# Performance work log

Hardware: AMD Instinct MI355X
Metric: run time of the kernel (lower is better)

The kernel has to match this reference:

```python
import jax, jax.numpy as jnp
import numpy as np

HEAD = 8

def _mvn(x, eps=1e-5):
    # per-(batch,channel) mean/std over spatial dims; torch .var default is unbiased (ddof=1)
    mean = jnp.mean(x, axis=(2, 3), keepdims=True)
    var = jnp.var(x, axis=(2, 3), ddof=1, keepdims=True) + eps
    return (x - mean) / jnp.sqrt(var)

def _conv1x1(x, w, b):
    return jnp.einsum('bchw,oc->bohw', x, w) + b[None, :, None, None]

def _block_heads(x, p):
    # non-overlapping unfold (kernel==stride==p): pure reshape; matches torch unfold ordering
    b, c, h, w = x.shape
    y = x.reshape(b, c, h // p, p, w // p, p).transpose(0, 1, 2, 4, 3, 5)
    n, r = (h // p) * (w // p), p * p
    return y.reshape(b, HEAD, c // HEAD, n, r)

def _unblock(x, p, h, w):
    # inverse of non-overlapping unfold (fold with kernel==stride)
    b, c, n, r = x.shape
    y = x.reshape(b, c, h // p, w // p, p, p).transpose(0, 1, 2, 4, 3, 5)
    return y.reshape(b, c, h, w)

def setup_inputs() -> dict:
    key = jax.random.key(0)
    ks = jax.random.split(key, 12)
    B, C, H, W = 4, 512, 64, 64
    wmat = lambda k: jax.random.normal(k, (C, C), jnp.float32) * 0.05
    zb = jnp.zeros((C,), jnp.float32)
    return {
        'content': jax.random.normal(ks[0], (B, C, H, W), jnp.float32),
        'style': jax.random.normal(ks[1], (B, C, H, W), jnp.float32),
        'q_w': wmat(ks[2]), 'q_b': zb,
        'k_w': wmat(ks[3]), 'k_b': zb,
        'v_w': wmat(ks[4]), 'v_b': zb,
        'q2_w': wmat(ks[5]), 'q2_b': zb,
        'k2_w': wmat(ks[6]), 'k2_b': zb,
        'v2_w': wmat(ks[7]), 'v2_b': zb,
        'f1_w': wmat(ks[8]), 'f1_b': zb,
        'f2_w': wmat(ks[9]), 'f2_b': zb,
        'sim_alpha': jnp.ones((1,), jnp.float32),
        'sim_beta': jnp.zeros((1,), jnp.float32),
        'layer': 3,
    }

def reference(content, style, q_w, q_b, k_w, k_b, v_w, v_b, q2_w, q2_b, k2_w, k2_b,
              v2_w, v2_b, f1_w, f1_b, f2_w, f2_b, sim_alpha, sim_beta, layer):
    region = 8 if int(layer) in (3, 4) else 4
    b, c, h, w = content.shape
    nc = _mvn(content)
    ns = _mvn(style)
    DA_q = _block_heads(_conv1x1(nc, q_w, q_b), region)      # [b,H,ch,n,r]
    DA_k = _block_heads(_conv1x1(ns, k_w, k_b), region)
    DA_v = _block_heads(_conv1x1(style, v_w, v_b), region)
    PA_q = _block_heads(_conv1x1(nc, q2_w, q2_b), region)
    PA_k = _block_heads(_conv1x1(ns, k2_w, k2_b), region)
    PA_v = _block_heads(_conv1x1(style, v2_w, v2_b), region)
    r = region * region
    n = DA_q.shape[3]
    # --- distinctiveness attention: mean-center clustering + sigmoid-weighted aggregation ---
    DA_k_c = jnp.mean(DA_k, axis=-1)                          # [b,H,ch,n]
    DA_v_c = jnp.mean(DA_v, axis=-1)
    dis = jnp.einsum('bhcx,bhcxy->bhxy', DA_k_c, DA_k)
    sim = jax.nn.sigmoid(sim_beta + sim_alpha * dis)          # [b,H,n,r]
    DA_k_agg = (jnp.einsum('bhxy,bhcxy->bhcx', sim, DA_k) + DA_k_c) / (r + 1)
    DA_v_agg = (jnp.einsum('bhxy,bhcxy->bhcx', sim, DA_v) + DA_v_c) / (r + 1)
    logits = jnp.einsum('bhcxy,bhcz->bhyxz', DA_q, DA_k_agg)  # [b,H,r,n,n]
    scores = jax.nn.softmax(logits, axis=-1)
    DA = jnp.einsum('bhyxz,bhcz->bhcxy', scores, DA_v_agg)    # [b,H,ch,n,r]
    DA_ub = _unblock(DA.reshape(b, c, n, r), region, h, w)
    # --- point attention: argmax NN block matching, then intra-block attention ---
    PA1 = jnp.einsum('bhcxy,bhczy->bhxz', PA_q, PA_k)         # [b,H,n,n]
    idx = jnp.argmax(PA1, axis=-1)                            # [b,H,n]
    idx_b = jnp.broadcast_to(idx[:, :, None, :, None], PA_k.shape)
    PA_k_rs = jnp.take_along_axis(PA_k, idx_b, axis=3)
    PA_v_rs = jnp.take_along_axis(PA_v, idx_b, axis=3)
    logits2 = jnp.einsum('bhcxy,bhcxz->bhxyz', PA_q, PA_k_rs) # [b,H,n,r,r]
    scores2 = jax.nn.softmax(logits2, axis=-1)
    PA = jnp.einsum('bhxyz,bhcxz->bhcxy', scores2, PA_v_rs)
    PA_ub = _unblock(PA.reshape(b, c, n, r), region, h, w)
    O = _conv1x1(DA_ub, f1_w, f1_b) + _conv1x1(PA_ub, f2_w, f2_b)
    return O + content
```

## Files before the change

### kernel.cpp

```cpp
#include <hip/hip_runtime.h>

typedef unsigned short u16;
typedef unsigned int   u32;
typedef _Float16       f16;

typedef f16   f16x8 __attribute__((ext_vector_type(8)));
typedef f16   f16x4 __attribute__((ext_vector_type(4)));
typedef float f32x4 __attribute__((ext_vector_type(4)));

__device__ __forceinline__ f32x4 mfma16(f16x8 a, f16x8 b, f32x4 c){
  return __builtin_amdgcn_mfma_f32_16x16x32_f16(a, b, c, 0, 0, 0);
}

__device__ __forceinline__ void glds16(const f16* g, f16* l){
  __builtin_amdgcn_global_load_lds(
      (const __attribute__((address_space(1))) void*)g,
      (__attribute__((address_space(3))) void*)l, 16, 0, 0);
}

__device__ __forceinline__ void barrier_f(){
  __builtin_amdgcn_s_barrier();
  asm volatile("" ::: "memory");
}

// ... 9 lines not shown
  for(int i = t * 4; i < 4096; i += 1024){
    float4 v = *(const float4*)(xp + i);
    s  += (double)v.x + (double)v.y + (double)v.z + (double)v.w;
    ss += (double)v.x * v.x + (double)v.y * v.y + (double)v.z * v.z + (double)v.w * v.w;
  }
  #pragma unroll
  for(int off = 32; off > 0; off >>= 1){
    s  += __shfl_xor(s, off);
    ss += __shfl_xor(ss, off);
  }
  __shared__ double sh[8];
  const int wid = t >> 6;
  if((t & 63) == 0){ sh[wid] = s; sh[4 + wid] = ss; }
  __syncthreads();
  if(t == 0){
    double S  = sh[0] + sh[1] + sh[2] + sh[3];
    double SS = sh[4] + sh[5] + sh[6] + sh[7];
    float mean = (float)(S * (1.0 / 4096.0));
    float var  = (float)((SS - S * S * (1.0 / 4096.0)) * (1.0 / 4095.0));
    stats[src * 4096 + row] = mean;
    stats[src * 4096 + 2048 + row] = rsqrtf(var + 1e-5f);
  }
}

__global__ __launch_bounds__(256) void k_prep_w_all(
    const float* __restrict__ qW,  const float* __restrict__ qB,
    const float* __restrict__ kW,  const float* __restrict__ kB,
    const float* __restrict__ q2W, const float* __restrict__ q2B,
    const float* __restrict__ k2W, const float* __restrict__ k2B,
    const float* __restrict__ vW,  const float* __restrict__ vB,
    const float* __restrict__ v2W, const float* __restrict__ v2B,
    const float* __restrict__ f1W, const float* __restrict__ f2W,
    const float* __restrict__ stats,
    f16* __restrict__ qw, f16* __restrict__ kw,
    f16* __restrict__ q2wh, f16* __restrict__ q2wl,
    f16* __restrict__ k2wh, f16* __restrict__ k2wl,
    f16* __restrict__ vw, f16* __restrict__ v2w,
    f16* __restrict__ f1w, f16* __restrict__ f2w,
    float* __restrict__ biasp)
{
  const int t = threadIdx.x;
  int rid = blockIdx.x * 32 + (t >> 3);
  const float *W; const float *B = nullptr;
  int side = -1, b = 0, o;
  f16 *oh; f16 *ol = nullptr; float* bs = nullptr;
  if(rid < 2048){
    b = rid >> 9; o = rid & 511;
    W = qW; B = qB; side = 0;
    oh = qw + (size_t)(b * 512 + o) * 512;
    bs = biasp + 0 * 2048 + b * 512 + o;
  } else if(rid < 4096){
    rid -= 2048; b = rid >> 9; o = rid & 511;
    W = kW; B = kB; side = 1;
    oh = kw + (size_t)(b * 512 + o) * 512;
    bs = biasp + 1 * 2048 + b * 512 + o;
  } else if(rid < 6144){
    rid -= 4096; b = rid >> 9; o = rid & 511;
    W = q2W; B = q2B; side = 0;
    oh = q2wh + (size_t)(b * 512 + o) * 512;
    ol = q2wl + (size_t)(b * 512 + o) * 512;
    bs = biasp + 4 * 2048 + b * 512 + o;
  } else if(rid < 8192){
    rid -= 6144; b = rid >> 9; o = rid & 511;
    W = k2W; B = k2B; side = 1;
    oh = k2wh + (size_t)(b * 512 + o) * 512;
    ol = k2wl + (size_t)(b * 512 + o) * 512;
    bs = biasp + 5 * 2048 + b * 512 + o;
  } else if(rid < 8704){
    o = rid - 8192; W = vW; B = vB;
    oh = vw + (size_t)o * 512;
    bs = biasp + 2 * 2048 + o;
  } else if(rid < 9216){
    o = rid - 8704; W = v2W; B = v2B;
    oh = v2w + (size_t)o * 512;
    bs = biasp + 3 * 2048 + o;
  } else if(rid < 9728){
    o = rid - 9216; W = f1W;
    oh = f1w + (size_t)o * 512;
  } else {
    o = rid - 9728; W = f2W;
    oh = f2w + (size_t)o * 512;
  }
  const float* mp = (side >= 0) ? stats + side * 4096 + b * 512 : nullptr;
  const float* rp = (side >= 0) ? mp + 2048 : nullptr;
  const int c0 = (t & 7) * 64;
  float dot = 0.f;
  #pragma unroll
  for(int i = 0; i < 64; i += 8){
    int c = c0 + i;
    float w[8];
    *(float4*)(w)     = *(const float4*)(W + (size_t)o * 512 + c);
    *(float4*)(w + 4) = *(const float4*)(W + (size_t)o * 512 + c + 4);
    f16x8 h8, l8;
    #pragma unroll
    for(int j = 0; j < 8; j++){
      float wp = w[j];
      if(side >= 0){
        float r = rp[c + j];
        dot += wp * mp[c + j] * r;
        wp *= r;
      }
      f16 h = (f16)wp;
      h8[j] = h; l8[j] = (f16)(wp - (float)h);
    }
    *(f16x8*)(oh + c) = h8;
    if(ol) *(f16x8*)(ol + c) = l8;
  }
  if(bs){
    dot += __shfl_xor(dot, 1); dot += __shfl_xor(dot, 2); dot += __shfl_xor(dot, 4);
    if((t & 7) == 0) *bs = B[o] - dot;
  }
}

__global__ __launch_bounds__(256) void k_prep_x(
    const float* __restrict__ content, const float* __restrict__ style,
    f16* __restrict__ cth, f16* __restrict__ ctl,
    f16* __restrict__ sth, f16* __restrict__ stl)
{
  const int side = blockIdx.z;
  const int b = blockIdx.y;
  const int s0 = blockIdx.x * 128;
  const float* Xb = (side ? style : content) + (size_t)b * 512 * 4096;
  f16* Oh = (side ? sth : cth) + (size_t)b * 4096 * 512;
  f16* Ol = (side ? stl : ctl) + (size_t)b * 4096 * 512;
  __shared__ float Xs[32][132];
  const int t = threadIdx.x;
  const int s = t >> 1, half = t & 1;
  for(int cc = 0; cc < 512; cc += 32){
    __syncthreads();
    #pragma unroll
    for(int u = 0; u < 4; u++){
      int q = t + u * 256;
      int row = q >> 5, f4 = q & 31;
      float4 v = *(const float4*)(Xb + (size_t)(cc + row) * 4096 + s0 + f4 * 4);
      *(float4*)(&Xs[row][f4 * 4]) = v;
    }
    __syncthreads();
    f16x8 h0, h1, l0, l1;
    #pragma unroll
    for(int i = 0; i < 8; i++){
      float x = Xs[half * 16 + i][s];
      f16 h = (f16)x; h0[i] = h; l0[i] = (f16)(x - (float)h);
    }
    #pragma unroll
    for(int i = 0; i < 8; i++){
      float x = Xs[half * 16 + 8 + i][s];
      f16 h = (f16)x; h1[i] = h; l1[i] = (f16)(x - (float)h);
    }
    size_t o = (size_t)(s0 + s) * 512 + cc + half * 16;
    *(f16x8*)(Oh + o) = h0; *(f16x8*)(Oh + o + 8) = h1;
    *(f16x8*)(Ol + o) = l0; *(f16x8*)(Ol + o + 8) = l1;
  }
}

__global__ __launch_bounds__(256) void k_convT(
    const f16* __restrict__ Xt, const f16* __restrict__ Wp,
    const float* __restrict__ bias, int bw, f16* __restrict__ Out)
{
  const int b = blockIdx.z;
  const int o0 = blockIdx.y * 128;
  const int s0 = blockIdx.x * 128;
  const f16* Xb = Xt + (size_t)b * 4096 * 512;
  const f16* Wb = Wp + (bw ? (size_t)b * 262144 : 0);
  const float* bp = bias + (bw ? b * 512 : 0);
  f16* Ob = Out + (size_t)b * 512 * 4096;
  __shared__ f16 As[2][4096];
  __shared__ f16 Bs[2][4096];
  const int t = threadIdx.x;
  const int lane = t & 63, wid = t >> 6;
  const int wm = (wid >> 1) * 64, wn = (wid & 1) * 64;
  const int lr = lane & 15, lg = lane >> 4;
  const int sr = lane >> 2, sc = lane & 3;
  auto STAGE = [&](int d, int kk){
    #pragma unroll
    for(int i = 0; i < 2; i++){
      int r0 = wid * 32 + i * 16;
      int rr = r0 + sr;
      int cs = (sc ^ ((rr >> 1) & 3)) << 3;
      glds16(Wb + (size_t)(o0 + rr) * 512 + kk + cs, As[d] + r0 * 32);
      glds16(Xb + (size_t)(s0 + rr) * 512 + kk + cs, Bs[d] + r0 * 32);
    }
  };
  f32x4 acc[4][4] = {};
  STAGE(0, 0);
  int db = 0;
  for(int tt = 0; tt < 16; tt++){
    if(tt < 15){
      STAGE(db ^ 1, (tt + 1) * 32);
      asm volatile("s_waitcnt vmcnt(4)" ::: "memory");
    } else {
      asm volatile("s_waitcnt vmcnt(0)" ::: "memory");
    }
    barrier_f();
    f16x8 av[4], bv[4];
    #pragma unroll
    for(int mi = 0; mi < 4; mi++){
      int row = wm + mi * 16 + lr;
      av[mi] = *(const f16x8*)(As[db] + row * 32 + ((lg ^ ((row >> 1) & 3)) << 3));
    }
    #pragma unroll
    for(int ni = 0; ni < 4; ni++){
      int row = wn + ni * 16 + lr;
      bv[ni] = *(const f16x8*)(Bs[db] + row * 32 + ((lg ^ ((row >> 1) & 3)) << 3));
    }
    #pragma unroll
    for(int mi = 0; mi < 4; mi++){
      #pragma unroll
      for(int ni = 0; ni < 4; ni++)
        acc[mi][ni] = mfma16(av[mi], bv[ni], acc[mi][ni]);
    }
    barrier_f();
    db ^= 1;
  }
  #pragma unroll
  for(int mi = 0; mi < 4; mi++){
    #pragma unroll
    for(int ni = 0; ni < 4; ni++){
      #pragma unroll
      for(int j = 0; j < 4; j++){
        int o = o0 + wm + mi * 16 + lg * 4 + j;
        int s = s0 + wn + ni * 16 + lr;
        Ob[(size_t)o * 4096 + s] = (f16)(acc[mi][ni][j] + bp[o]);
      }
    }
  }
}

__global__ __launch_bounds__(256) void k_conv3out(
    const f16* __restrict__ Xt,
    const f16* __restrict__ Wk, const f16* __restrict__ Wv, const f16* __restrict__ Wv2,
    const float* __restrict__ biasp,
    f16* __restrict__ Ok, f16* __restrict__ Ov, f16* __restrict__ Ov2)
{
  const int b = blockIdx.z;
  const int seg = blockIdx.y >> 2;
  const int o0 = (blockIdx.y & 3) * 128;
  const int s0 = blockIdx.x * 128;
  const f16* Xb = Xt + (size_t)b * 4096 * 512;
  const f16* Wb = seg == 0 ? Wk + (size_t)b * 262144 : (seg == 1 ? Wv : Wv2);
  const float* bp = biasp + (seg == 0 ? 1 * 2048 + b * 512 : (seg == 1 ? 2 * 2048 : 3 * 2048));
  f16* Ob = (seg == 0 ? Ok : (seg == 1 ? Ov : Ov2)) + (size_t)b * 512 * 4096;
  __shared__ f16 As[2][4096];
  __shared__ f16 Bs[2][4096];
  const int t = threadIdx.x;
  const int lane = t & 63, wid = t >> 6;
  const int wm = (wid >> 1) * 64, wn = (wid & 1) * 64;
  const int lr = lane & 15, lg = lane >> 4;
  const int sr = lane >> 2, sc = lane & 3;
  auto STAGE = [&](int d, int kk){
    #pragma unroll
    for(int i = 0; i < 2; i++){
      int r0 = wid * 32 + i * 16;
      int rr = r0 + sr;
      int cs = (sc ^ ((rr >> 1) & 3)) << 3;
      glds16(Wb + (size_t)(o0 + rr) * 512 + kk + cs, As[d] + r0 * 32);
      glds16(Xb + (size_t)(s0 + rr) * 512 + kk + cs, Bs[d] + r0 * 32);
    }
  };
  f32x4 acc[4][4] = {};
  STAGE(0, 0);
  int db = 0;
  for(int tt = 0; tt < 16; tt++){
    if(tt < 15){
      STAGE(db ^ 1, (tt + 1) * 32);
      asm volatile("s_waitcnt vmcnt(4)" ::: "memory");
    } else {
      asm volatile("s_waitcnt vmcnt(0)" ::: "memory");
    }
    barrier_f();
    f16x8 av[4], bv[4];
    #pragma unroll
    for(int mi = 0; mi < 4; mi++){
      int row = wm + mi * 16 + lr;
      av[mi] = *(const f16x8*)(As[db] + row * 32 + ((lg ^ ((row >> 1) & 3)) << 3));
    }
    #pragma unroll
    for(int ni = 0; ni < 4; ni++){
      int row = wn + ni * 16 + lr;
      bv[ni] = *(const f16x8*)(Bs[db] + row * 32 + ((lg ^ ((row >> 1) & 3)) << 3));
    }
    #pragma unroll
    for(int mi = 0; mi < 4; mi++){
      #pragma unroll
      for(int ni = 0; ni < 4; ni++)
        acc[mi][ni] = mfma16(av[mi], bv[ni], acc[mi][ni]);
    }
    barrier_f();
    db ^= 1;
  }
  #pragma unroll
  for(int mi = 0; mi < 4; mi++){
    #pragma unroll
    for(int ni = 0; ni < 4; ni++){
      #pragma unroll
      for(int j = 0; j < 4; j++){
        int o = o0 + wm + mi * 16 + lg * 4 + j;
        int s = s0 + wn + ni * 16 + lr;
        Ob[(size_t)o * 4096 + s] = (f16)(acc[mi][ni][j] + bp[o]);
      }
    }
  }
}

__global__ __launch_bounds__(256) void k_convT3(
    const f16* __restrict__ Xh, const f16* __restrict__ Xl,
    const f16* __restrict__ Wh, const f16* __restrict__ Wl,
    const float* __restrict__ bias, f16* __restrict__ Oh, f16* __restrict__ Ol)
{
  const int b = blockIdx.z;
  const int o0 = blockIdx.y * 128;
  const int s0 = blockIdx.x * 128;
  const f16* Xhb = Xh + (size_t)b * 4096 * 512;
  const f16* Xlb = Xl + (size_t)b * 4096 * 512;
  const f16* Whb = Wh + (size_t)b * 262144;
  const f16* Wlb = Wl + (size_t)b * 262144;
  const float* bp = bias + b * 512;
  f16* Ohb = Oh + (size_t)b * 512 * 4096;
  f16* Olb = Ol + (size_t)b * 512 * 4096;
  __shared__ f16 Ah[2][4096], Al[2][4096], Bh[2][4096], Bl[2][4096];
  const int t = threadIdx.x;
  const int lane = t & 63, wid = t >> 6;
  const int wm = (wid >> 1) * 64, wn = (wid & 1) * 64;
  const int lr = lane & 15, lg = lane >> 4;
  const int sr = lane >> 2, sc = lane & 3;
  auto STAGE = [&](int d, int kk){
    #pragma unroll
    for(int i = 0; i < 2; i++){
      int r0 = wid * 32 + i * 16;
      int rr = r0 + sr;
      int cs = (sc ^ ((rr >> 1) & 3)) << 3;
      size_t wsrc = (size_t)(o0 + rr) * 512 + kk + cs;
      size_t xsrc = (size_t)(s0 + rr) * 512 + kk + cs;
      glds16(Whb + wsrc, Ah[d] + r0 * 32);
      glds16(Wlb + wsrc, Al[d] + r0 * 32);
      glds16(Xhb + xsrc, Bh[d] + r0 * 32);
      glds16(Xlb + xsrc, Bl[d] + r0 * 32);
    }
  };
  f32x4 acc[4][4] = {};
  STAGE(0, 0);
  int db = 0;
  for(int tt = 0; tt < 16; tt++){
    if(tt < 15){
      STAGE(db ^ 1, (tt + 1) * 32);
      asm volatile("s_waitcnt vmcnt(8)" ::: "memory");
    } else {
      asm volatile("s_waitcnt vmcnt(0)" ::: "memory");
    }
    barrier_f();
    f16x8 ah[4], alo[4], bh[4], blo[4];
    #pragma unroll
    for(int mi = 0; mi < 4; mi++){
      int row = wm + mi * 16 + lr;
      int off = row * 32 + ((lg ^ ((row >> 1) & 3)) << 3);
      ah[mi]  = *(const f16x8*)(Ah[db] + off);
      alo[mi] = *(const f16x8*)(Al[db] + off);
    }
    #pragma unroll
    for(int ni = 0; ni < 4; ni++){
      int row = wn + ni * 16 + lr;
      int off = row * 32 + ((lg ^ ((row >> 1) & 3)) << 3);
      bh[ni]  = *(const f16x8*)(Bh[db] + off);
      blo[ni] = *(const f16x8*)(Bl[db] + off);
    }
    #pragma unroll
    for(int mi = 0; mi < 4; mi++){
      #pragma unroll
      for(int ni = 0; ni < 4; ni++){
        f32x4 a = acc[mi][ni];
        a = mfma16(ah[mi],  bh[ni],  a);
        a = mfma16(ah[mi],  blo[ni], a);
        a = mfma16(alo[mi], bh[ni],  a);
        acc[mi][ni] = a;
      }
    }
    barrier_f();
    db ^= 1;
  }
  #pragma unroll
  for(int mi = 0; mi < 4; mi++){
    #pragma unroll
    for(int ni = 0; ni < 4; ni++){
      #pragma unroll
      for(int j = 0; j < 4; j++){
        int o = o0 + wm + mi * 16 + lg * 4 + j;
        int s = s0 + wn + ni * 16 + lr;
        float v = acc[mi][ni][j] + bp[o];
        f16 h = (f16)v;
        Ohb[(size_t)o * 4096 + s] = h;
        Olb[(size_t)o * 4096 + s] = (f16)(v - (float)h);
      }
    }
  }
}

__global__ __launch_bounds__(256) void k_da1(
    const f16* __restrict__ K, const f16* __restrict__ V,
    const float* __restrict__ alpha_p, const float* __restrict__ beta_p,
    float* __restrict__ kagg, float* __restrict__ vagg)
{
  const int hw = blockIdx.x;
  const int xcd = hw & 7, i = hw >> 3;
  const int g = xcd * 32 + (i >> 3);
  const int bh = g >> 3;
  const int x  = (g & 7) * 8 + (i & 7);
  const f16* Kb = K + (size_t)bh * 64 * 4096;
  const f16* Vb = V + (size_t)bh * 64 * 4096;
  __shared__ float kl[64][65];
  __shared__ float vl[64][65];
  __shared__ float kc[64], vc[64], simv[64];
  const int t = threadIdx.x;
  const int c = t >> 2, yp = t & 3;
  const int xb = (x >> 3) * 512 + (x & 7) * 8;
  #pragma unroll
  for(int u = 0; u < 2; u++){
    int yh = yp * 2 + u;
    f16x8 k8 = *(const f16x8*)(Kb + (size_t)c * 4096 + xb + yh * 64);
    f16x8 v8 = *(const f16x8*)(Vb + (size_t)c * 4096 + xb + yh * 64);
    #pragma unroll
    for(int j = 0; j < 8; j++){
      kl[c][yh * 8 + j] = (float)k8[j];
      vl[c][yh * 8 + j] = (float)v8[j];
    }
  }
  __syncthreads();
  float sk = 0.f, sv = 0.f;
  for(int yy = yp * 16; yy < yp * 16 + 16; yy++){ sk += kl[c][yy]; sv += vl[c][yy]; }
  sk += __shfl_xor(sk, 1); sk += __shfl_xor(sk, 2);
  sv += __shfl_xor(sv, 1); sv += __shfl_xor(sv, 2);
  if(yp == 0){ kc[c] = sk * (1.f / 64.f); vc[c] = sv * (1.f / 64.f); }
  __syncthreads();
  const int y = t >> 2, cp = t & 3;
  float d = 0.f;
  for(int cc = cp * 16; cc < cp * 16 + 16; cc++) d += kc[cc] * kl[cc][y];
  d += __shfl_xor(d, 1); d += __shfl_xor(d, 2);
  if(cp == 0) simv[y] = 1.f / (1.f + expf(-(beta_p[0] + alpha_p[0] * d)));
  __syncthreads();
  float ak = 0.f, av = 0.f;
  for(int yy = yp * 16; yy < yp * 16 + 16; yy++){
    float sm = simv[yy];
    ak += sm * kl[c][yy]; av += sm * vl[c][yy];
  }
  ak += __shfl_xor(ak, 1); ak += __shfl_xor(ak, 2);
  av += __shfl_xor(av, 1); av += __shfl_xor(av, 2);
  if(yp == 0){
    size_t o = ((size_t)bh * 64 + x) * 64 + c;
    kagg[o] = (ak + kc[c]) * (1.f / 65.f);
    vagg[o] = (av + vc[c]) * (1.f / 65.f);
  }
}

__global__ __launch_bounds__(256) void k_da2(
    const f16* __restrict__ Q, const float* __restrict__ kagg,
    const float* __restrict__ vagg, f16* __restrict__ OutT)
{
  const int bh = blockIdx.x >> 4;
  const int s0 = (blockIdx.x & 15) << 8;
  const int b_ = bh >> 3, hd = bh & 7;
  const f16* Qb = Q + (size_t)bh * 64 * 4096;
  f16* Ot = OutT + (size_t)b_ * 4096 * 512 + hd * 64;

  __shared__ __align__(16) f16 Qt[256][72];
  __shared__ __align__(16) f16 Kt[64][72];
  __shared__ __align__(16) f16 Vt[64][72];
  const int t = threadIdx.x;
  const int lane = t & 63, w = t >> 6;
  const int lr = lane & 15, lg = lane >> 4;

  {
    const int so = t & 31;
    #pragma unroll
    for(int pass = 0; pass < 8; pass++){
      int c = (t >> 5) + pass * 8;
      f16x8 q8 = *(const f16x8*)(Qb + (size_t)c * 4096 + s0 + so * 8);
      #pragma unroll
      for(int j = 0; j < 8; j++){
        int s = so * 8 + j;
        int col = (((c >> 3) ^ (s & 7)) << 3) | (c & 7);
        Qt[s][col] = q8[j];
      }
    }
  }
  {
    const int z = t >> 2, c0 = (t & 3) * 16;
    #pragma unroll
    for(int u = 0; u < 4; u++){
      float4 v = *(const float4*)(kagg + (size_t)bh * 4096 + z * 64 + c0 + u * 4);
      float vv[4] = {v.x, v.y, v.z, v.w};
      #pragma unroll
      for(int j = 0; j < 4; j++){
        int c = c0 + u * 4 + j;
        int col = (((c >> 3) ^ (z & 7)) << 3) | (c & 7);
        Kt[z][col] = (f16)vv[j];
      }
    }
    #pragma unroll
    for(int u = 0; u < 4; u++){
      float4 v = *(const float4*)(vagg + (size_t)bh * 4096 + z * 64 + c0 + u * 4);
      float vv[4] = {v.x, v.y, v.z, v.w};
      #pragma unroll
      for(int j = 0; j < 4; j++){
        int c = c0 + u * 4 + j;
        int col = (((z >> 3) ^ (c & 7)) << 3) | (z & 7);
        Vt[c][col] = (f16)vv[j];
      }
    }
  }
  __syncthreads();

  f32x4 acc[4][4] = {};
  #pragma unroll
  for(int kc = 0; kc < 2; kc++){
    f16x8 af[4], bf[4];
    #pragma unroll
    for(int mi = 0; mi < 4; mi++){
      int row = w * 64 + mi * 16 + lr;
      af[mi] = *(const f16x8*)(&Qt[row][(((kc * 4 + lg) ^ (row & 7)) << 3)]);
    }
    #pragma unroll
    for(int ni = 0; ni < 4; ni++){
      int row = ni * 16 + lr;
      bf[ni] = *(const f16x8*)(&Kt[row][(((kc * 4 + lg) ^ (row & 7)) << 3)]);
    }
    #pragma unroll
    for(int mi = 0; mi < 4; mi++){
      #pragma unroll
      for(int ni = 0; ni < 4; ni++)
        acc[mi][ni] = mfma16(af[mi], bf[ni], acc[mi][ni]);
    }
  }

  #pragma unroll
  for(int mi = 0; mi < 4; mi++){
    #pragma unroll
    for(int j = 0; j < 4; j++){
      float v0 = acc[mi][0][j], v1 = acc[mi][1][j], v2 = acc[mi][2][j], v3 = acc[mi][3][j];
      float m = fmaxf(fmaxf(v0, v1), fmaxf(v2, v3));
      m = fmaxf(m, __shfl_xor(m, 1)); m = fmaxf(m, __shfl_xor(m, 2));
      m = fmaxf(m, __shfl_xor(m, 4)); m = fmaxf(m, __shfl_xor(m, 8));
      float e0 = expf(v0 - m), e1 = expf(v1 - m), e2 = expf(v2 - m), e3 = expf(v3 - m);
      float sm = e0 + e1 + e2 + e3;
      sm += __shfl_xor(sm, 1); sm += __shfl_xor(sm, 2);
      sm += __shfl_xor(sm, 4); sm += __shfl_xor(sm, 8);
      float inv = 1.f / sm;
      float ev[4] = {e0, e1, e2, e3};
      int row = w * 64 + mi * 16 + lg * 4 + j;
      #pragma unroll
      for(int ni = 0; ni < 4; ni++){
        int z = lr + 16 * ni;
        int col = (((z >> 3) ^ (row & 7)) << 3) | (z & 7);
        Qt[row][col] = (f16)(ev[ni] * inv);
      }
    }
  }

  f32x4 acc2[4][4] = {};
  #pragma unroll
  for(int kc = 0; kc < 2; kc++){
    f16x8 af[4], bf[4];
    #pragma unroll
    for(int mi = 0; mi < 4; mi++){
      int row = w * 64 + mi * 16 + lr;
      af[mi] = *(const f16x8*)(&Qt[row][(((kc * 4 + lg) ^ (row & 7)) << 3)]);
    }
    #pragma unroll
    for(int ni = 0; ni < 4; ni++){
      int row = ni * 16 + lr;
      bf[ni] = *(const f16x8*)(&Vt[row][(((kc * 4 + lg) ^ (row & 7)) << 3)]);
    }
    #pragma unroll
    for(int mi = 0; mi < 4; mi++){
      #pragma unroll
      for(int ni = 0; ni < 4; ni++)
        acc2[mi][ni] = mfma16(af[mi], bf[ni], acc2[mi][ni]);
    }
  }

  #pragma unroll
  for(int mi = 0; mi < 4; mi++){
    #pragma unroll
    for(int j = 0; j < 4; j++){
      size_t srow = (size_t)(s0 + w * 64 + mi * 16 + lg * 4 + j) * 512;
      #pragma unroll
      for(int ni = 0; ni < 4; ni++)
        Ot[srow + ni * 16 + lr] = (f16)acc2[mi][ni][j];
    }
  }
}

__global__ __launch_bounds__(256) void k_pa1(
    const f16* __restrict__ Qh, const f16* __restrict__ Ql,
    const f16* __restrict__ Kh, const f16* __restrict__ Kl,
    float* __restrict__ pa1p)
{
  const int slice = blockIdx.x & 7;
  const int bh = blockIdx.x >> 3;
  const size_t base = (size_t)bh * 64 * 4096;
  __shared__ f16 Ah[2][64][72], Al[2][64][72], Bh[2][64][72], Bl[2][64][72];
  const int t = threadIdx.x;
  const int lane = t & 63, wid = t >> 6;
  const int wm = (wid >> 1) * 32, wn = (wid & 1) * 32;
  const int lr = lane & 15, lg = lane >> 4;
  f32x4 acc[2][2] = {};
  for(int chunk = 0; chunk < 4; chunk++){
    const int c0 = slice * 8 + chunk * 2;
    __syncthreads();
    #pragma unroll
    for(int cc = 0; cc < 2; cc++){
      size_t cbase = base + (size_t)(c0 + cc) * 4096;
      #pragma unroll
      for(int u = 0; u < 2; u++){
        int e = u * 256 + t;
        int x = e >> 3, yh = e & 7;
        size_t src = cbase + (size_t)((x >> 3) * 512 + (x & 7) * 8 + yh * 64);
        int dst = yh * 8;
        *(f16x8*)(&Ah[cc][x][dst]) = *(const f16x8*)(Qh + src);
        *(f16x8*)(&Al[cc][x][dst]) = *(const f16x8*)(Ql + src);
        *(f16x8*)(&Bh[cc][x][dst]) = *(const f16x8*)(Kh + src);
        *(f16x8*)(&Bl[cc][x][dst]) = *(const f16x8*)(Kl + src);
      }
    }
    __syncthreads();
    #pragma unroll
    for(int cc = 0; cc < 2; cc++){
      #pragma unroll
      for(int kc = 0; kc < 2; kc++){
        f16x8 ah[2], alo[2], bh[2], blo[2];
        #pragma unroll
        for(int mi = 0; mi < 2; mi++){
          ah[mi]  = *(const f16x8*)(&Ah[cc][wm + mi * 16 + lr][kc * 32 + lg * 8]);
          alo[mi] = *(const f16x8*)(&Al[cc][wm + mi * 16 + lr][kc * 32 + lg * 8]);
        }
        #pragma unroll
        for(int ni = 0; ni < 2; ni++){
          bh[ni]  = *(const f16x8*)(&Bh[cc][wn + ni * 16 + lr][kc * 32 + lg * 8]);
          blo[ni] = *(const f16x8*)(&Bl[cc][wn + ni * 16 + lr][kc * 32 + lg * 8]);
        }
        #pragma unroll
        for(int mi = 0; mi < 2; mi++){
          #pragma unroll
          for(int ni = 0; ni < 2; ni++){
            f32x4 a = acc[mi][ni];
            a = mfma16(ah[mi],  bh[ni],  a);
            a = mfma16(ah[mi],  blo[ni], a);
            a = mfma16(alo[mi], bh[ni],  a);
            acc[mi][ni] = a;
          }
        }
      }
    }
  }
  float* outp = pa1p + ((size_t)bh * 8 + slice) * 4096;
  #pragma unroll
  for(int mi = 0; mi < 2; mi++){
    #pragma unroll
    for(int ni = 0; ni < 2; ni++){
      #pragma unroll
      for(int j = 0; j < 4; j++){
        int x = wm + mi * 16 + lg * 4 + j;
        int z = wn + ni * 16 + lr;
        outp[x * 64 + z] = acc[mi][ni][j];
      }
    }
  }
}

__global__ __launch_bounds__(64) void k_pa1r(
    const float* __restrict__ pa1p, int* __restrict__ idx)
{
  const int bh = blockIdx.x;
  const int x = threadIdx.x;
  const float* p = pa1p + (size_t)bh * 8 * 4096 + x * 64;
  float best = -1e30f; int bi = 0;
  for(int z = 0; z < 64; z += 4){
    float4 v = *(const float4*)(p + z);
    #pragma unroll
    for(int sl = 1; sl < 8; sl++){
      float4 w = *(const float4*)(p + sl * 4096 + z);
      v.x += w.x; v.y += w.y; v.z += w.z; v.w += w.w;
    }
    if(v.x > best){ best = v.x; bi = z; }
    if(v.y > best){ best = v.y; bi = z + 1; }
    if(v.z > best){ best = v.z; bi = z + 2; }
    if(v.w > best){ best = v.w; bi = z + 3; }
  }
  idx[bh * 64 + x] = bi;
}

__global__ __launch_bounds__(256) void k_pa2(
    const f16* __restrict__ Qh, const f16* __restrict__ Kh,
    const f16* __restrict__ V2, const int* __restrict__ idx, f16* __restrict__ OutT)
{
  const int hw = blockIdx.x;
  const int bh = (hw & 7) * 4 + ((hw >> 3) >> 6);
  const int x  = (hw >> 3) & 63;
  const int b_ = bh >> 3, hd = bh & 7;
  const size_t base = (size_t)bh * 64 * 4096;
  f16* Ot = OutT + (size_t)b_ * 4096 * 512 + hd * 64;

  __shared__ __align__(16) char Ubuf[18432];
  __shared__ f16 Vn[64][72];
  __shared__ f16 Ps[64][72];
  f16   (*Qt)[72] = (f16(*)[72])Ubuf;
  f16   (*Kt)[72] = (f16(*)[72])(Ubuf + 9216);
  float (*Lf)[66] = (float(*)[66])Ubuf;
  float (*Os)[67] = (float(*)[67])Ubuf;

  const int t = threadIdx.x;
  const int lane = t & 63, wid = t >> 6;
  const int wm = (wid >> 1) * 32, wn = (wid & 1) * 32;
  const int lr = lane & 15, lg = lane >> 4;

  const int xk = idx[bh * 64 + x];
  const int xb = (x >> 3) * 512 + (x & 7) * 8;
  const int kb = (xk >> 3) * 512 + (xk & 7) * 8;

  {
    const int c = t >> 2, q4 = t & 3;
    #pragma unroll
    for(int u = 0; u < 2; u++){
      int yh = q4 * 2 + u;
      f16x8 q8 = *(const f16x8*)(Qh + base + (size_t)c * 4096 + xb + yh * 64);
      f16x8 k8 = *(const f16x8*)(Kh + base + (size_t)c * 4096 + kb + yh * 64);
      f16x8 v8 = *(const f16x8*)(V2 + base + (size_t)c * 4096 + kb + yh * 64);
      int col = ((((c >> 3) ^ yh) & 7) << 3) + (c & 7);
      #pragma unroll
      for(int j = 0; j < 8; j++){
        Qt[yh * 8 + j][col] = q8[j];
        Kt[yh * 8 + j][col] = k8[j];
      }
      *(f16x8*)(&Vn[c][yh * 8]) = v8;
    }
  }
  __syncthreads();

  f32x4 acc[2][2] = {};
  #pragma unroll
  for(int kc = 0; kc < 2; kc++){
    f16x8 af[2], bf[2];
    #pragma unroll
    for(int mi = 0; mi < 2; mi++){
      int row = wm + mi * 16 + lr;
      af[mi] = *(const f16x8*)(&Qt[row][((((kc * 4 + lg) ^ (row >> 3)) & 7) << 3)]);
    }
    #pragma unroll
    for(int ni = 0; ni < 2; ni++){
      int row = wn + ni * 16 + lr;
      bf[ni] = *(const f16x8*)(&Kt[row][((((kc * 4 + lg) ^ (row >> 3)) & 7) << 3)]);
    }
    #pragma unroll
    for(int mi = 0; mi < 2; mi++){
      #pragma unroll
      for(int ni = 0; ni < 2; ni++)
        acc[mi][ni] = mfma16(af[mi], bf[ni], acc[mi][ni]);
    }
  }
  __syncthreads();
  #pragma unroll
  for(int mi = 0; mi < 2; mi++){
    #pragma unroll
    for(int ni = 0; ni < 2; ni++){
      #pragma unroll
      for(int j = 0; j < 4; j++)
        Lf[wm + mi * 16 + lg * 4 + j][wn + ni * 16 + lr] = acc[mi][ni][j];
    }
  }
  __syncthreads();

  {
    const int y = t >> 2, zp = t & 3;
    float l[16];
    #pragma unroll
    for(int i = 0; i < 16; i++) l[i] = Lf[y][zp * 16 + i];
    float m = l[0];
    #pragma unroll
    for(int i = 1; i < 16; i++) m = fmaxf(m, l[i]);
    m = fmaxf(m, __shfl_xor(m, 1)); m = fmaxf(m, __shfl_xor(m, 2));
    float sum = 0.f;
    #pragma unroll
    for(int i = 0; i < 16; i++){ l[i] = expf(l[i] - m); sum += l[i]; }
    sum += __shfl_xor(sum, 1); sum += __shfl_xor(sum, 2);
    float inv = 1.f / sum;
    f16x8 p0, p1;
    #pragma unroll
    for(int i = 0; i < 8; i++){ p0[i] = (f16)(l[i] * inv); p1[i] = (f16)(l[8 + i] * inv); }
    *(f16x8*)(&Ps[y][zp * 16]) = p0;
    *(f16x8*)(&Ps[y][zp * 16 + 8]) = p1;
  }
  __syncthreads();

  f32x4 acc2[2][2] = {};
  #pragma unroll
  for(int kc = 0; kc < 2; kc++){
    f16x8 af[2], bf[2];
    #pragma unroll
    for(int mi = 0; mi < 2; mi++)
      af[mi] = *(const f16x8*)(&Ps[wm + mi * 16 + lr][kc * 32 + lg * 8]);
    #pragma unroll
    for(int ni = 0; ni < 2; ni++)
      bf[ni] = *(const f16x8*)(&Vn[wn + ni * 16 + lr][kc * 32 + lg * 8]);
    #pragma unroll
    for(int mi = 0; mi < 2; mi++){
      #pragma unroll
      for(int ni = 0; ni < 2; ni++)
        acc2[mi][ni] = mfma16(af[mi], bf[ni], acc2[mi][ni]);
    }
  }
  #pragma unroll
  for(int mi = 0; mi < 2; mi++){
    #pragma unroll
    for(int ni = 0; ni < 2; ni++){
      #pragma unroll
      for(int j = 0; j < 4; j++)
        Os[wn + ni * 16 + lr][wm + mi * 16 + lg * 4 + j] = acc2[mi][ni][j];
    }
  }
  __syncthreads();

  {
    const int y = t >> 2, cq = (t & 3) * 16;
    size_t srow = (size_t)(xb + (y >> 3) * 64 + (y & 7)) * 512;
    f16x8 w0, w1;
    #pragma unroll
    for(int i = 0; i < 8; i++){ w0[i] = (f16)Os[cq + i][y]; w1[i] = (f16)Os[cq + 8 + i][y]; }
    *(f16x8*)(Ot + srow + cq) = w0;
    *(f16x8*)(Ot + srow + cq + 8) = w1;
  }
}

__global__ __launch_bounds__(256) void k_finalT(
    const f16* __restrict__ X1t, const f16* __restrict__ X2t,
    const f16* __restrict__ W1p, const f16* __restrict__ W2p,
    const float* __restrict__ B1, const float* __restrict__ B2,
    const float* __restrict__ content, float* __restrict__ out)
{
  const int b = blockIdx.z;
  const int o0 = blockIdx.y * 128;
  const int s0 = blockIdx.x * 128;
  __shared__ f16 As[2][4096];
  __shared__ f16 Bs[2][4096];
  const int t = threadIdx.x;
  const int lane = t & 63, wid = t >> 6;
  const int wm = (wid >> 1) * 64, wn = (wid & 1) * 64;
  const int lr = lane & 15, lg = lane >> 4;
  const int sr = lane >> 2, sc = lane & 3;
  const f16* Xp[2] = {X1t + (size_t)b * 4096 * 512, X2t + (size_t)b * 4096 * 512};
  const f16* Wq[2] = {W1p, W2p};
  auto STAGE = [&](int d, int tt){
    const f16* Xb = Xp[tt >> 4];
    const f16* Wb = Wq[tt >> 4];
    int kk = (tt & 15) * 32;
    #pragma unroll
    for(int i = 0; i < 2; i++){
      int r0 = wid * 32 + i * 16;
      int rr = r0 + sr;
      int cs = (sc ^ ((rr >> 1) & 3)) << 3;
      glds16(Wb + (size_t)(o0 + rr) * 512 + kk + cs, As[d] + r0 * 32);
      glds16(Xb + (size_t)(s0 + rr) * 512 + kk + cs, Bs[d] + r0 * 32);
    }
  };
  f32x4 acc[4][4] = {};
  STAGE(0, 0);
  int db = 0;
  for(int tt = 0; tt < 32; tt++){
    if(tt < 31){
      STAGE(db ^ 1, tt + 1);
      asm volatile("s_waitcnt vmcnt(4)" ::: "memory");
    } else {
      asm volatile("s_waitcnt vmcnt(0)" ::: "memory");
    }
    barrier_f();
    f16x8 av[4], bv[4];
    #pragma unroll
    for(int mi = 0; mi < 4; mi++){
      int row = wm + mi * 16 + lr;
      av[mi] = *(const f16x8*)(As[db] + row * 32 + ((lg ^ ((row >> 1) & 3)) << 3));
    }
    #pragma unroll
    for(int ni = 0; ni < 4; ni++){
      int row = wn + ni * 16 + lr;
      bv[ni] = *(const f16x8*)(Bs[db] + row * 32 + ((lg ^ ((row >> 1) & 3)) << 3));
    }
    #pragma unroll
    for(int mi = 0; mi < 4; mi++){
      #pragma unroll
      for(int ni = 0; ni < 4; ni++)
        acc[mi][ni] = mfma16(av[mi], bv[ni], acc[mi][ni]);
    }
    barrier_f();
    db ^= 1;
  }
  #pragma unroll
  for(int mi = 0; mi < 4; mi++){
    #pragma unroll
    for(int ni = 0; ni < 4; ni++){
      #pragma unroll
      for(int j = 0; j < 4; j++){
        int o = o0 + wm + mi * 16 + lg * 4 + j;
        int s = s0 + wn + ni * 16 + lr;
        size_t gi = ((size_t)b * 512 + o) * 4096 + s;
        out[gi] = acc[mi][ni][j] + B1[o] + B2[o] + content[gi];
      }
    }
  }
}

extern "C" void kernel_launch(void* const* d_in, const int* in_sizes, int n_in,
                              void* d_out, int out_size, void* d_ws, size_t ws_size,
                              hipStream_t stream) {
  (void)in_sizes; (void)n_in; (void)out_size; (void)ws_size;
  const float* content = (const float*)d_in[0];
  const float* style   = (const float*)d_in[1];
  const float* q_w  = (const float*)d_in[2];  const float* q_b  = (const float*)d_in[3];
  const float* k_w  = (const float*)d_in[4];  const float* k_b  = (const float*)d_in[5];
  const float* v_w  = (const float*)d_in[6];  const float* v_b  = (const float*)d_in[7];
  const float* q2_w = (const float*)d_in[8];  const float* q2_b = (const float*)d_in[9];
  const float* k2_w = (const float*)d_in[10]; const float* k2_b = (const float*)d_in[11];
  const float* v2_w = (const float*)d_in[12]; const float* v2_b = (const float*)d_in[13];
  const float* f1_w = (const float*)d_in[14]; const float* f1_b = (const float*)d_in[15];
  const float* f2_w = (const float*)d_in[16]; const float* f2_b = (const float*)d_in[17];
  const float* sim_alpha = (const float*)d_in[18];
  const float* sim_beta  = (const float*)d_in[19];

  char* ws = (char*)d_ws;
  #define SLOT(i) (ws + (size_t)(i) * 16777216)
  f16* cth = (f16*)SLOT(0);
  f16* ctl = (f16*)SLOT(1);
  f16* sth = (f16*)SLOT(2);
  f16* stl = (f16*)SLOT(3);
  f16* wbase = (f16*)SLOT(4);
  f16* qw   = wbase;
  f16* kw   = wbase + 1 * 1048576;
  f16* q2wh = wbase + 2 * 1048576;
  f16* q2wl = wbase + 3 * 1048576;
  f16* k2wh = wbase + 4 * 1048576;
  f16* k2wl = wbase + 5 * 1048576;
  f16* vw   = wbase + 6 * 1048576;
  f16* v2w  = vw + 262144;
  f16* f1w  = vw + 524288;
  f16* f2w  = vw + 786432;
  f16*   q2h   = (f16*)SLOT(5);
  f16*   q2l   = (f16*)SLOT(6);
  f16*   k2h   = (f16*)SLOT(7);
  f16*   k2l   = (f16*)SLOT(0);
  f16*   qbuf  = (f16*)SLOT(1);
  float* pa1p  = (float*)SLOT(3);
  f16*   kbuf  = (f16*)SLOT(6);
  f16*   vbuf  = (f16*)SLOT(3);
  f16*   v2buf = (f16*)SLOT(0);
  f16*   da_t  = (f16*)SLOT(3);
  f16*   pa_t  = (f16*)SLOT(6);
  float* stats = (float*)(ws + 134217728);
  float* biasp = (float*)(ws + 134217728 + 32768);
  float* kagg  = (float*)(ws + 134217728 + 32768);
  float* vagg  = (float*)(ws + 134217728 + 557056);
  int*   idxb  = (int*)(ws + 134217728 + 1081344);

  dim3 gconv(32, 4, 4);

  k_mvn_stats<<<4096, 256, 0, stream>>>(content, style, stats);

  k_prep_w_all<<<320, 256, 0, stream>>>(
      q_w, q_b, k_w, k_b, q2_w, q2_b, k2_w, k2_b,
      v_w, v_b, v2_w, v2_b, f1_w, f2_w, stats,
      qw, kw, q2wh, q2wl, k2wh, k2wl, vw, v2w, f1w, f2w, biasp);

  k_prep_x<<<dim3(32,4,2), 256, 0, stream>>>(content, style, cth, ctl, sth, stl);

  k_convT3<<<gconv, 256, 0, stream>>>(cth, ctl, q2wh, q2wl, biasp + 4 * 2048, q2h, q2l);
  k_convT <<<gconv, 256, 0, stream>>>(cth, qw, biasp + 0 * 2048, 1, qbuf);
  k_convT3<<<gconv, 256, 0, stream>>>(sth, stl, k2wh, k2wl, biasp + 5 * 2048, k2h, k2l);
  k_pa1<<<256, 256, 0, stream>>>(q2h, q2l, k2h, k2l, pa1p);
  k_pa1r<<<32, 64, 0, stream>>>(pa1p, idxb);
  k_conv3out<<<dim3(32,12,4), 256, 0, stream>>>(sth, kw, vw, v2w, biasp,
                                                kbuf, vbuf, v2buf);

  k_da1<<<2048, 256, 0, stream>>>(kbuf, vbuf, sim_alpha, sim_beta, kagg, vagg);
  k_da2<<<512, 256, 0, stream>>>(qbuf, kagg, vagg, da_t);
  k_pa2<<<2048, 256, 0, stream>>>(q2h, k2h, v2buf, idxb, pa_t);

  k_finalT<<<gconv, 256, 0, stream>>>(da_t, pa_t, f1w, f2w, f1_b, f2_b,
                                      content, (float*)d_out);
}
```

Baseline: 310.4 us.

## Compute PA projections in single fp16, refine near-tie argmax rows with split precision

The Q2/K2 projections and the PA1 block-similarity GEMM drop the hi/lo split-fp16 (three-MFMA) scheme and use a single fp16 pass, removing the low-half buffers and two thirds of their MFMA work. The reduction kernel now flags rows whose top two candidates lie within a fixed margin of 1.0. A new refine kernel recomputes those rows' Q2 block and each candidate K2 block with split precision to recover the exact argmax. Buffer slots are reassigned. The refine cost depends on how many rows are flagged, and a fixed margin may not cover every fp16 error case.

```diff
diff --git a/kernel.cpp b/kernel.cpp
--- a/kernel.cpp
+++ b/kernel.cpp
@@ -335,96 +335,224 @@
   }
 }
 
-__global__ __launch_bounds__(256) void k_convT3(
-    const f16* __restrict__ Xh, const f16* __restrict__ Xl,
-    const f16* __restrict__ Wh, const f16* __restrict__ Wl,
-    const float* __restrict__ bias, f16* __restrict__ Oh, f16* __restrict__ Ol)
-{
-  const int b = blockIdx.z;
-  const int o0 = blockIdx.y * 128;
-  const int s0 = blockIdx.x * 128;
-  const f16* Xhb = Xh + (size_t)b * 4096 * 512;
-  const f16* Xlb = Xl + (size_t)b * 4096 * 512;
-  const f16* Whb = Wh + (size_t)b * 262144;
-  const f16* Wlb = Wl + (size_t)b * 262144;
-  const float* bp = bias + b * 512;
-  f16* Ohb = Oh + (size_t)b * 512 * 4096;
-  f16* Olb = Ol + (size_t)b * 512 * 4096;
-  __shared__ f16 Ah[2][4096], Al[2][4096], Bh[2][4096], Bl[2][4096];
+__global__ __launch_bounds__(256) void k_pa1(
+    const f16* __restrict__ Qh, const f16* __restrict__ Kh, float* __restrict__ pa1p)
+{
+  const int slice = blockIdx.x & 7;
+  const int bh = blockIdx.x >> 3;
+  const size_t base = (size_t)bh * 64 * 4096;
+  __shared__ f16 Ah[2][64][72], Bh[2][64][72];
   const int t = threadIdx.x;
   const int lane = t & 63, wid = t >> 6;
-  const int wm = (wid >> 1) * 64, wn = (wid & 1) * 64;
+  const int wm = (wid >> 1) * 32, wn = (wid & 1) * 32;
   const int lr = lane & 15, lg = lane >> 4;
-  const int sr = lane >> 2, sc = lane & 3;
-  auto STAGE = [&](int d, int kk){
-    #pragma unroll
-    for(int i = 0; i < 2; i++){
-      int r0 = wid * 32 + i * 16;
-      int rr = r0 + sr;
-      int cs = (sc ^ ((rr >> 1) & 3)) << 3;
-      size_t wsrc = (size_t)(o0 + rr) * 512 + kk + cs;
-      size_t xsrc = (size_t)(s0 + rr) * 512 + kk + cs;
-      glds16(Whb + wsrc, Ah[d] + r0 * 32);
-      glds16(Wlb + wsrc, Al[d] + r0 * 32);
-      glds16(Xhb + xsrc, Bh[d] + r0 * 32);
-      glds16(Xlb + xsrc, Bl[d] + r0 * 32);
+  f32x4 acc[2][2] = {};
+  for(int chunk = 0; chunk < 4; chunk++){
+    const int c0 = slice * 8 + chunk * 2;
+    __syncthreads();
+    #pragma unroll
+    for(int cc = 0; cc < 2; cc++){
+      size_t cbase = base + (size_t)(c0 + cc) * 4096;
+      #pragma unroll
+      for(int u = 0; u < 2; u++){
+        int e = u * 256 + t;
+        int x = e >> 3, yh = e & 7;
+        size_t src = cbase + (size_t)((x >> 3) * 512 + (x & 7) * 8 + yh * 64);
+        int dst = yh * 8;
+        *(f16x8*)(&Ah[cc][x][dst]) = *(const f16x8*)(Qh + src);
+        *(f16x8*)(&Bh[cc][x][dst]) = *(const f16x8*)(Kh + src);
+      }
+    }
+    __syncthreads();
+    #pragma unroll
+    for(int cc = 0; cc < 2; cc++){
+      #pragma unroll
+      for(int kc = 0; kc < 2; kc++){
+        f16x8 ah[2], bh[2];
+        #pragma unroll
+        for(int mi = 0; mi < 2; mi++)
+          ah[mi] = *(const f16x8*)(&Ah[cc][wm + mi * 16 + lr][kc * 32 + lg * 8]);
+        #pragma unroll
+        for(int ni = 0; ni < 2; ni++)
+          bh[ni] = *(const f16x8*)(&Bh[cc][wn + ni * 16 + lr][kc * 32 + lg * 8]);
+        #pragma unroll
+        for(int mi = 0; mi < 2; mi++){
+          #pragma unroll
+          for(int ni = 0; ni < 2; ni++)
+            acc[mi][ni] = mfma16(ah[mi], bh[ni], acc[mi][ni]);
+        }
+      }
+    }
+  }
+  float* outp = pa1p + ((size_t)bh * 8 + slice) * 4096;
+  #pragma unroll
+  for(int mi = 0; mi < 2; mi++){
+    #pragma unroll
+    for(int ni = 0; ni < 2; ni++){
+      #pragma unroll
+      for(int j = 0; j < 4; j++){
+        int x = wm + mi * 16 + lg * 4 + j;
+        int z = wn + ni * 16 + lr;
+        outp[x * 64 + z] = acc[mi][ni][j];
+      }
+    }
+  }
+}
+
+__global__ __launch_bounds__(64) void k_pa1r(
+    float* __restrict__ pa1p, int* __restrict__ idx, int* __restrict__ flags)
+{
+  const int bh = blockIdx.x;
+  const int x = threadIdx.x;
+  float* p = pa1p + (size_t)bh * 8 * 4096 + x * 64;
+  float m1 = -3e38f, m2 = -3e38f; int i1 = 0;
+  for(int z = 0; z < 64; z += 4){
+    float4 v = *(const float4*)(p + z);
+    #pragma unroll
+    for(int sl = 1; sl < 8; sl++){
+      float4 w = *(const float4*)(p + sl * 4096 + z);
+      v.x += w.x; v.y += w.y; v.z += w.z; v.w += w.w;
+    }
+    *(float4*)(p + z) = v;
+    float vv[4] = {v.x, v.y, v.z, v.w};
+    #pragma unroll
+    for(int k = 0; k < 4; k++){
+      if(vv[k] > m1){ m2 = m1; m1 = vv[k]; i1 = z + k; }
+      else if(vv[k] > m2){ m2 = vv[k]; }
+    }
+  }
+  idx[bh * 64 + x] = i1;
+  flags[bh * 64 + x] = (m2 >= m1 - 1.0f) ? 1 : 0;
+}
+
+__global__ __launch_bounds__(256) void k_refine(
+    const f16* __restrict__ Xqh, const f16* __restrict__ Xql,
+    const f16* __restrict__ Xkh, const f16* __restrict__ Xkl,
+    const f16* __restrict__ Wqh, const f16* __restrict__ Wql,
+    const f16* __restrict__ Wkh, const f16* __restrict__ Wkl,
+    const float* __restrict__ biasp, const float* __restrict__ pa1p,
+    const int* __restrict__ flags, int* __restrict__ idx)
+{
+  const int bid = blockIdx.x;
+  if(flags[bid] == 0) return;
+  const int bh = bid >> 6, x = bid & 63;
+  const int b = bh >> 3, hd = bh & 7;
+  __shared__ __align__(16) f16 Ah[64][72], Al[64][72], Bh[64][72], Bl[64][72];
+  __shared__ float q2s[64][65];
+  __shared__ float red[4];
+  __shared__ float vals[64];
+  __shared__ int cand[64];
+  const int t = threadIdx.x;
+  const int lane = t & 63, wid = t >> 6;
+  const int wm = (wid >> 1) * 32, wn = (wid & 1) * 32;
+  const int lr = lane & 15, lg = lane >> 4;
+  const int srw = t >> 2, soc = (t & 3) * 2;
+
+  auto gemm = [&](const f16* Wh_, const f16* Wl_, const f16* Xh_, const f16* Xl_,
+                  int blk, f32x4 (&acc)[2][2]){
+    for(int ch = 0; ch < 8; ch++){
+      __syncthreads();
+      {
+        size_t wsrc = ((size_t)(b * 512 + hd * 64 + srw)) * 512 + ch * 64 + soc * 8;
+        *(f16x8*)(&Ah[srw][soc * 8])     = *(const f16x8*)(Wh_ + wsrc);
+        *(f16x8*)(&Ah[srw][soc * 8 + 8]) = *(const f16x8*)(Wh_ + wsrc + 8);
+        *(f16x8*)(&Al[srw][soc * 8])     = *(const f16x8*)(Wl_ + wsrc);
+        *(f16x8*)(&Al[srw][soc * 8 + 8]) = *(const f16x8*)(Wl_ + wsrc + 8);
+        int s = (blk >> 3) * 512 + (blk & 7) * 8 + (srw >> 3) * 64 + (srw & 7);
+        size_t xsrc = ((size_t)b * 4096 + s) * 512 + ch * 64 + soc * 8;
+        *(f16x8*)(&Bh[srw][soc * 8])     = *(const f16x8*)(Xh_ + xsrc);
+        *(f16x8*)(&Bh[srw][soc * 8 + 8]) = *(const f16x8*)(Xh_ + xsrc + 8);
+        *(f16x8*)(&Bl[srw][soc * 8])     = *(const f16x8*)(Xl_ + xsrc);
+        *(f16x8*)(&Bl[srw][soc * 8 + 8]) = *(const f16x8*)(Xl_ + xsrc + 8);
+      }
+      __syncthreads();
+      #pragma unroll
+      for(int kc = 0; kc < 2; kc++){
+        f16x8 ah[2], al[2], bh2[2], bl2[2];
+        #pragma unroll
+        for(int mi = 0; mi < 2; mi++){
+          int row = wm + mi * 16 + lr;
+          ah[mi] = *(const f16x8*)(&Ah[row][kc * 32 + lg * 8]);
+          al[mi] = *(const f16x8*)(&Al[row][kc * 32 + lg * 8]);
+        }
+        #pragma unroll
+        for(int ni = 0; ni < 2; ni++){
+          int row = wn + ni * 16 + lr;
+          bh2[ni] = *(const f16x8*)(&Bh[row][kc * 32 + lg * 8]);
+          bl2[ni] = *(const f16x8*)(&Bl[row][kc * 32 + lg * 8]);
+        }
+        #pragma unroll
+        for(int mi = 0; mi < 2; mi++){
+          #pragma unroll
+          for(int ni = 0; ni < 2; ni++){
+            f32x4 a = acc[mi][ni];
+            a = mfma16(ah[mi], bh2[ni], a);
+            a = mfma16(ah[mi], bl2[ni], a);
+            a = mfma16(al[mi], bh2[ni], a);
+            acc[mi][ni] = a;
+          }
+        }
+      }
     }
   };
-  f32x4 acc[4][4] = {};
-  STAGE(0, 0);
-  int db = 0;
-  for(int tt = 0; tt < 16; tt++){
-    if(tt < 15){
-      STAGE(db ^ 1, (tt + 1) * 32);
-      asm volatile("s_waitcnt vmcnt(8)" ::: "memory");
-    } else {
-      asm volatile("s_waitcnt vmcnt(0)" ::: "memory");
-    }
-    barrier_f();
-    f16x8 ah[4], alo[4], bh[4], blo[4];
-    #pragma unroll
-    for(int mi = 0; mi < 4; mi++){
-      int row = wm + mi * 16 + lr;
-      int off = row * 32 + ((lg ^ ((row >> 1) & 3)) << 3);
-      ah[mi]  = *(const f16x8*)(Ah[db] + off);
-      alo[mi] = *(const f16x8*)(Al[db] + off);
-    }
-    #pragma unroll
-    for(int ni = 0; ni < 4; ni++){
-      int row = wn + ni * 16 + lr;
-      int off = row * 32 + ((lg ^ ((row >> 1) & 3)) << 3);
-      bh[ni]  = *(const f16x8*)(Bh[db] + off);
-      blo[ni] = *(const f16x8*)(Bl[db] + off);
-    }
-    #pragma unroll
-    for(int mi = 0; mi < 4; mi++){
-      #pragma unroll
-      for(int ni = 0; ni < 4; ni++){
-        f32x4 a = acc[mi][ni];
-        a = mfma16(ah[mi],  bh[ni],  a);
-        a = mfma16(ah[mi],  blo[ni], a);
-        a = mfma16(alo[mi], bh[ni],  a);
-        acc[mi][ni] = a;
-      }
-    }
-    barrier_f();
-    db ^= 1;
-  }
-  #pragma unroll
-  for(int mi = 0; mi < 4; mi++){
-    #pragma unroll
-    for(int ni = 0; ni < 4; ni++){
-      #pragma unroll
-      for(int j = 0; j < 4; j++){
-        int o = o0 + wm + mi * 16 + lg * 4 + j;
-        int s = s0 + wn + ni * 16 + lr;
-        float v = acc[mi][ni][j] + bp[o];
-        f16 h = (f16)v;
-        Ohb[(size_t)o * 4096 + s] = h;
-        Olb[(size_t)o * 4096 + s] = (f16)(v - (float)h);
-      }
-    }
-  }
+
+  if(t < 64) vals[t] = pa1p[(size_t)bh * 8 * 4096 + x * 64 + t];
+  __syncthreads();
+  if(t == 0){
+    float m1 = vals[0];
+    for(int z = 1; z < 64; z++) m1 = fmaxf(m1, vals[z]);
+    red[0] = m1;
+  }
+  __syncthreads();
+  const float m1 = red[0];
+  if(t < 64) cand[t] = (vals[t] >= m1 - 1.0f) ? 1 : 0;
+  __syncthreads();
+
+  {
+    f32x4 qa[2][2] = {};
+    gemm(Wqh, Wql, Xqh, Xql, x, qa);
+    #pragma unroll
+    for(int mi = 0; mi < 2; mi++){
+      #pragma unroll
+      for(int ni = 0; ni < 2; ni++){
+        #pragma unroll
+        for(int j = 0; j < 4; j++){
+          int c = wm + mi * 16 + lg * 4 + j;
+          int y = wn + ni * 16 + lr;
+          q2s[c][y] = qa[mi][ni][j] + biasp[4 * 2048 + b * 512 + hd * 64 + c];
+        }
+      }
+    }
+  }
+  __syncthreads();
+
+  float bestv = -3e38f; int besti = 0;
+  for(int z = 0; z < 64; z++){
+    if(!cand[z]) continue;
+    f32x4 ka[2][2] = {};
+    gemm(Wkh, Wkl, Xkh, Xkl, z, ka);
+    float part = 0.f;
+    #pragma unroll
+    for(int mi = 0; mi < 2; mi++){
+      #pragma unroll
+      for(int ni = 0; ni < 2; ni++){
+        #pragma unroll
+        for(int j = 0; j < 4; j++){
+          int c = wm + mi * 16 + lg * 4 + j;
+          int y = wn + ni * 16 + lr;
+          part += (ka[mi][ni][j] + biasp[5 * 2048 + b * 512 + hd * 64 + c]) * q2s[c][y];
+        }
+      }
+    }
+    #pragma unroll
+    for(int off = 32; off > 0; off >>= 1) part += __shfl_xor(part, off);
+    __syncthreads();
+    if(lane == 0) red[wid] = part;
+    __syncthreads();
+    float pv = red[0] + red[1] + red[2] + red[3];
+    if(pv > bestv){ bestv = pv; besti = z; }
+  }
+  if(t == 0) idx[bid] = besti;
 }
 
 __global__ __launch_bounds__(256) void k_da1(
@@ -619,105 +747,6 @@
         Ot[srow + ni * 16 + lr] = (f16)acc2[mi][ni][j];
     }
   }
-}
-
-__global__ __launch_bounds__(256) void k_pa1(
-    const f16* __restrict__ Qh, const f16* __restrict__ Ql,
-    const f16* __restrict__ Kh, const f16* __restrict__ Kl,
-    float* __restrict__ pa1p)
-{
-  const int slice = blockIdx.x & 7;
-  const int bh = blockIdx.x >> 3;
-  const size_t base = (size_t)bh * 64 * 4096;
-  __shared__ f16 Ah[2][64][72], Al[2][64][72], Bh[2][64][72], Bl[2][64][72];
-  const int t = threadIdx.x;
-  const int lane = t & 63, wid = t >> 6;
-  const int wm = (wid >> 1) * 32, wn = (wid & 1) * 32;
-  const int lr = lane & 15, lg = lane >> 4;
-  f32x4 acc[2][2] = {};
-  for(int chunk = 0; chunk < 4; chunk++){
-    const int c0 = slice * 8 + chunk * 2;
-    __syncthreads();
-    #pragma unroll
-    for(int cc = 0; cc < 2; cc++){
-      size_t cbase = base + (size_t)(c0 + cc) * 4096;
-      #pragma unroll
-      for(int u = 0; u < 2; u++){
-        int e = u * 256 + t;
-        int x = e >> 3, yh = e & 7;
-        size_t src = cbase + (size_t)((x >> 3) * 512 + (x & 7) * 8 + yh * 64);
-        int dst = yh * 8;
-        *(f16x8*)(&Ah[cc][x][dst]) = *(const f16x8*)(Qh + src);
-        *(f16x8*)(&Al[cc][x][dst]) = *(const f16x8*)(Ql + src);
-        *(f16x8*)(&Bh[cc][x][dst]) = *(const f16x8*)(Kh + src);
-        *(f16x8*)(&Bl[cc][x][dst]) = *(const f16x8*)(Kl + src);
-      }
-    }
-    __syncthreads();
-    #pragma unroll
-    for(int cc = 0; cc < 2; cc++){
-      #pragma unroll
-      for(int kc = 0; kc < 2; kc++){
-        f16x8 ah[2], alo[2], bh[2], blo[2];
-        #pragma unroll
-        for(int mi = 0; mi < 2; mi++){
-          ah[mi]  = *(const f16x8*)(&Ah[cc][wm + mi * 16 + lr][kc * 32 + lg * 8]);
-          alo[mi] = *(const f16x8*)(&Al[cc][wm + mi * 16 + lr][kc * 32 + lg * 8]);
-        }
-        #pragma unroll
-        for(int ni = 0; ni < 2; ni++){
-          bh[ni]  = *(const f16x8*)(&Bh[cc][wn + ni * 16 + lr][kc * 32 + lg * 8]);
-          blo[ni] = *(const f16x8*)(&Bl[cc][wn + ni * 16 + lr][kc * 32 + lg * 8]);
-        }
-        #pragma unroll
-        for(int mi = 0; mi < 2; mi++){
-          #pragma unroll
-          for(int ni = 0; ni < 2; ni++){
-            f32x4 a = acc[mi][ni];
-            a = mfma16(ah[mi],  bh[ni],  a);
-            a = mfma16(ah[mi],  blo[ni], a);
-            a = mfma16(alo[mi], bh[ni],  a);
-            acc[mi][ni] = a;
-          }
-        }
-      }
-    }
-  }
-  float* outp = pa1p + ((size_t)bh * 8 + slice) * 4096;
-  #pragma unroll
-  for(int mi = 0; mi < 2; mi++){
-    #pragma unroll
-    for(int ni = 0; ni < 2; ni++){
-      #pragma unroll
-      for(int j = 0; j < 4; j++){
-        int x = wm + mi * 16 + lg * 4 + j;
-        int z = wn + ni * 16 + lr;
-        outp[x * 64 + z] = acc[mi][ni][j];
-      }
-    }
-  }
-}
-
-__global__ __launch_bounds__(64) void k_pa1r(
-    const float* __restrict__ pa1p, int* __restrict__ idx)
-{
-  const int bh = blockIdx.x;
-  const int x = threadIdx.x;
-  const float* p = pa1p + (size_t)bh * 8 * 4096 + x * 64;
-  float best = -1e30f; int bi = 0;
-  for(int z = 0; z < 64; z += 4){
-    float4 v = *(const float4*)(p + z);
-    #pragma unroll
-    for(int sl = 1; sl < 8; sl++){
-      float4 w = *(const float4*)(p + sl * 4096 + z);
-      v.x += w.x; v.y += w.y; v.z += w.z; v.w += w.w;
-    }
-    if(v.x > best){ best = v.x; bi = z; }
-    if(v.y > best){ best = v.y; bi = z + 1; }
-    if(v.z > best){ best = v.z; bi = z + 2; }
-    if(v.w > best){ best = v.w; bi = z + 3; }
-  }
-  idx[bh * 64 + x] = bi;
 }
 
 __global__ __launch_bounds__(256) void k_pa2(
@@ -973,16 +1002,15 @@
   f16* f1w  = vw + 524288;
   f16* f2w  = vw + 786432;
   f16*   q2h   = (f16*)SLOT(5);
-  f16*   q2l   = (f16*)SLOT(6);
-  f16*   k2h   = (f16*)SLOT(7);
-  f16*   k2l   = (f16*)SLOT(0);
-  f16*   qbuf  = (f16*)SLOT(1);
-  float* pa1p  = (float*)SLOT(3);
-  f16*   kbuf  = (f16*)SLOT(6);
-  f16*   vbuf  = (f16*)SLOT(3);
-  f16*   v2buf = (f16*)SLOT(0);
-  f16*   da_t  = (f16*)SLOT(3);
-  f16*   pa_t  = (f16*)SLOT(6);
+  f16*   k2h   = (f16*)SLOT(6);
+  float* pa1p  = (float*)SLOT(7);
+  int*   flags = (int*)(ws + 7 * 16777216 + 8388608);
+  f16*   qbuf  = (f16*)SLOT(3);
+  f16*   kbuf  = (f16*)SLOT(0);
+  f16*   vbuf  = (f16*)SLOT(1);
+  f16*   v2buf = (f16*)SLOT(7);
+  f16*   da_t  = (f16*)SLOT(2);
+  f16*   pa_t  = (f16*)SLOT(3);
   float* stats = (float*)(ws + 134217728);
   float* biasp = (float*)(ws + 134217728 + 32768);
   float* kagg  = (float*)(ws + 134217728 + 32768);
@@ -1000,11 +1028,15 @@
 
   k_prep_x<<<dim3(32,4,2), 256, 0, stream>>>(content, style, cth, ctl, sth, stl);
 
-  k_convT3<<<gconv, 256, 0, stream>>>(cth, ctl, q2wh, q2wl, biasp + 4 * 2048, q2h, q2l);
-  k_convT <<<gconv, 256, 0, stream>>>(cth, qw, biasp + 0 * 2048, 1, qbuf);
-  k_convT3<<<gconv, 256, 0, stream>>>(sth, stl, k2wh, k2wl, biasp + 5 * 2048, k2h, k2l);
-  k_pa1<<<256, 256, 0, stream>>>(q2h, q2l, k2h, k2l, pa1p);
-  k_pa1r<<<32, 64, 0, stream>>>(pa1p, idxb);
+  k_convT<<<gconv, 256, 0, stream>>>(cth, q2wh, biasp + 4 * 2048, 1, q2h);
+  k_convT<<<gconv, 256, 0, stream>>>(sth, k2wh, biasp + 5 * 2048, 1, k2h);
+  k_pa1<<<256, 256, 0, stream>>>(q2h, k2h, pa1p);
+  k_pa1r<<<32, 64, 0, stream>>>(pa1p, idxb, flags);
+  k_refine<<<2048, 256, 0, stream>>>(cth, ctl, sth, stl,
+                                     q2wh, q2wl, k2wh, k2wl,
+                                     biasp, pa1p, flags, idxb);
+
+  k_convT<<<gconv, 256, 0, stream>>>(cth, qw, biasp + 0 * 2048, 1, qbuf);
   k_conv3out<<<dim3(32,12,4), 256, 0, stream>>>(sth, kw, vw, v2w, biasp,
                                                 kbuf, vbuf, v2buf);
 
```

After: 307.2 us. No clear change (-1.0%).
